# Performance work log

Hardware: AMD Instinct MI355X
Metric: run time of the kernel (lower is better)

The kernel has to match this reference:

```python
import jax, jax.numpy as jnp
import numpy as np

PAD_ID = 0    # scibert [PAD]
SEP_ID = 103  # scibert [SEP]
IGNORE = 100


def setup_inputs() -> dict:
    key = jax.random.key(0)
    ks = jax.random.split(key, 8)
    B, S, D, T = 64, 512, 768, 2
    return {
        "sequence_output": jax.random.normal(ks[0], (B, S, D), dtype=jnp.float32),
        "input_ids": jax.random.randint(ks[1], (B, S), 0, 31090, dtype=jnp.int64),
        "labels": jax.random.randint(ks[2], (B, S), 0, 2, dtype=jnp.int64),
        "W": jax.random.normal(ks[3], (T, D), dtype=jnp.float32) * 0.02,
        "b": jax.random.normal(ks[4], (T,), dtype=jnp.float32) * 0.02,
        "start_trans": jax.random.normal(ks[5], (T,), dtype=jnp.float32) * 0.1,
        "end_trans": jax.random.normal(ks[6], (T,), dtype=jnp.float32) * 0.1,
        "trans": jax.random.normal(ks[7], (T, T), dtype=jnp.float32) * 0.1,
    }


def _crf_llh_token_mean(em, tags, start, end, trans):
    # em: [B,S,T], tags: [B,S]; mask=None in torchcrf => all-ones mask.
    B, S, T = em.shape
    # numerator: score of the gold path
    em_tag = jnp.take_along_axis(em, tags[..., None], axis=2)[..., 0]        # [B,S]
    tr_tag = trans[tags[:, :-1], tags[:, 1:]]                                 # [B,S-1]
    score = start[tags[:, 0]] + em_tag.sum(1) + tr_tag.sum(1) + end[tags[:, -1]]
    # denominator: forward algorithm over time (scan over S-1 tiny steps)
    alpha0 = start[None, :] + em[:, 0]                                        # [B,T]
    em_rest = jnp.swapaxes(em[:, 1:], 0, 1)                                   # [S-1,B,T]

    def step(alpha, em_t):
        # alpha[b,i] + trans[i,j] + em_t[b,j] -> logsumexp over i
        nxt = jax.nn.logsumexp(alpha[:, :, None] + trans[None], axis=1) + em_t
        return nxt, None

    alpha, _ = jax.lax.scan(step, alpha0, em_rest)
    logZ = jax.nn.logsumexp(alpha + end[None, :], axis=1)                     # [B]
    llh = score - logZ
    # reduction='token_mean' with all-ones mask -> sum / (B*S)
    return llh.sum() / jnp.float32(B * S)


def _crf_viterbi(em, start, end, trans):
    # em: [B,S,T] -> decoded tags [B,S] int32
    B, S, T = em.shape
    score0 = start[None, :] + em[:, 0]                                        # [B,T]
    em_rest = jnp.swapaxes(em[:, 1:], 0, 1)                                   # [S-1,B,T]

    def vstep(score, em_t):
        cand = score[:, :, None] + trans[None] + em_t[:, None, :]             # [B,T,T]
        return cand.max(axis=1), cand.argmax(axis=1).astype(jnp.int32)

    final, hist = jax.lax.scan(vstep, score0, em_rest)                        # hist [S-1,B,T]
    final = final + end[None, :]
    last = jnp.argmax(final, axis=1).astype(jnp.int32)                        # [B]

    def back(tag, bp_t):
        prev = jnp.take_along_axis(bp_t, tag[:, None], axis=1)[:, 0]
        return prev, prev

    _, prevs = jax.lax.scan(back, last, hist, reverse=True)                   # [S-1,B]
    tags = jnp.concatenate([prevs, last[None, :]], axis=0)                    # [S,B]
    return jnp.swapaxes(tags, 0, 1)                                           # [B,S]


def reference(sequence_output, input_ids, labels, W, b, start_trans, end_trans, trans):
    mask = (input_ids != PAD_ID) & (input_ids != SEP_ID) & (labels != IGNORE)  # [B,S] bool
    seq = sequence_output * mask[..., None].astype(sequence_output.dtype)
    labels_m = labels * mask.astype(labels.dtype)
    # probablities = relu(hidden2tag(seq))
    em = jax.nn.relu(jnp.einsum("bsd,td->bst", seq, W) + b)                    # [B,S,2]
    loss = _crf_llh_token_mean(em, labels_m, start_trans, end_trans, trans)
    target_emissions = _crf_viterbi(em, start_trans, end_trans, trans).astype(jnp.float32)
    return (loss, target_emissions, labels_m, mask)
```

## Files before the change

### kernel.cpp

```cpp
#include <hip/hip_runtime.h>

#define BB 64
#define SS 512
#define DD 768
#define NROWS (BB*SS)
#define NEG (-1e30f)

__global__ __launch_bounds__(256) void k_emissions(
    const float* __restrict__ seq,
    const int*   __restrict__ input_ids,
    const int*   __restrict__ labels,
    const float* __restrict__ W,
    const float* __restrict__ bias,
    float* __restrict__ em_t,
    int*   __restrict__ tags_t,
    float* __restrict__ out)
{
    const int lane = threadIdx.x & 63;
    const int wid  = blockIdx.x * 4 + (threadIdx.x >> 6);
    const int base = wid * 4;

    const float4* W4 = (const float4*)W;
    float4 w0[3], w1[3];
#pragma unroll
    for (int j = 0; j < 3; ++j) {
        w0[j] = W4[j*64 + lane];
        w1[j] = W4[192 + j*64 + lane];
    }
    const float b0 = bias[0], b1 = bias[1];

    const float4* s4 = (const float4*)seq;
    float4 v[4][3];
#pragma unroll
    for (int r = 0; r < 4; ++r)
#pragma unroll
        for (int j = 0; j < 3; ++j)
            v[r][j] = s4[(size_t)(base + r)*192 + j*64 + lane];

    float d0[4], d1[4];
#pragma unroll
    for (int r = 0; r < 4; ++r) {
        float a0 = 0.f, a1 = 0.f;
#pragma unroll
        for (int j = 0; j < 3; ++j) {
            float4 x = v[r][j];
            a0 += x.x*w0[j].x + x.y*w0[j].y + x.z*w0[j].z + x.w*w0[j].w;
            a1 += x.x*w1[j].x + x.y*w1[j].y + x.z*w1[j].z + x.w*w1[j].w;
        }
        d0[r] = a0; d1[r] = a1;
    }
#pragma unroll
    for (int m = 32; m >= 1; m >>= 1) {
#pragma unroll
        for (int r = 0; r < 4; ++r) {
            d0[r] += __shfl_xor(d0[r], m, 64);
            d1[r] += __shfl_xor(d1[r], m, 64);
        }
    }
    if (lane == 0) {
        const int4 idv = *(const int4*)(input_ids + base);
        const int4 lbv = *(const int4*)(labels + base);
        const int ida[4] = {idv.x, idv.y, idv.z, idv.w};
        const int lba[4] = {lbv.x, lbv.y, lbv.z, lbv.w};
#pragma unroll
        for (int r = 0; r < 4; ++r) {
            const int row = base + r;
            const int id = ida[r], lab = lba[r];
            const int msk = (id != 0 && id != 103 && lab != 100) ? 1 : 0;
            const int lm  = lab * msk;
            const float e0 = fmaxf((msk ? d0[r] : 0.f) + b0, 0.f);
            const float e1 = fmaxf((msk ? d1[r] : 0.f) + b1, 0.f);
            const int b_ = row >> 9, s_ = row & 511;
            *(float2*)(em_t + (s_*BB + b_)*2) = make_float2(e0, e1);
            tags_t[s_*BB + b_] = lm;
            out[1 + NROWS   + row] = (float)lm;
            out[1 + 2*NROWS + row] = (float)msk;
        }
    }
}

__device__ __forceinline__ float lse2(float x, float y) {
    float m = fmaxf(x, y);
    float d = fminf(x, y) - m;
    return m + __logf(1.f + __expf(d));
}

__global__ __launch_bounds__(512) void k_crf(
    const float* __restrict__ em_t,
    const int*   __restrict__ tags_t,
    const float* __restrict__ start,
    const float* __restrict__ endt,
    const float* __restrict__ trans,
    float* __restrict__ out)
{
    __shared__ float4 logP4[8][64];
    __shared__ float4 vitP4[8][64];
    __shared__ float  scoreP[8][64];
    __shared__ float2 vbound[8][64];
    __shared__ unsigned char last_tag_sh[64];
    __shared__ unsigned int  bp_sh[64*33];
    __shared__ unsigned char tags_sh[64*516];

    const int tid  = threadIdx.x;
    const int lane = tid & 63;
    const int wv   = tid >> 6;
    const float t00 = trans[0], t01 = trans[1], t10 = trans[2], t11 = trans[3];
    const float s0 = start[0], s1 = start[1];
    const float e0 = endt[0],  e1 = endt[1];
    const float2* em2 = (const float2*)em_t;

    {
        const int b = lane, c = wv;
        const int k0 = c * 64;
        float2 emv = em2[k0*64 + b];
        int    tg  = tags_t[k0*64 + b];
        float P00,P01,P10,P11, V00,V01,V10,V11, score;
        if (c == 0) {
            P00 = 0.f; P01 = NEG; P10 = NEG; P11 = 0.f;
            V00 = 0.f; V01 = NEG; V10 = NEG; V11 = 0.f;
            score = tg ? (s1 + emv.y) : (s0 + emv.x);
        } else {
            int pt = tags_t[(k0-1)*64 + b];
            P00 = t00 + emv.x; P01 = t01 + emv.y;
            P10 = t10 + emv.x; P11 = t11 + emv.y;
            V00 = P00; V01 = P01; V10 = P10; V11 = P11;
            score = (pt ? (tg ? t11 : t10) : (tg ? t01 : t00))
                  + (tg ? emv.y : emv.x);
        }
        int ptag = tg;

        float2 eb[21]; int tb[21];
#pragma unroll
        for (int i = 0; i < 21; ++i) {
            int kp = k0 + 1 + i;
            eb[i] = em2[kp*64 + b];
            tb[i] = tags_t[kp*64 + b];
        }
#pragma unroll
        for (int jb = 0; jb < 3; ++jb) {
#pragma unroll
            for (int i = 0; i < 21; ++i) {
                const int k = k0 + 1 + jb*21 + i;
                float2 em = eb[i]; int tag = tb[i];
                int kp = k + 21; if (kp > 511) kp = 511;
                eb[i] = em2[kp*64 + b];
                tb[i] = tags_t[kp*64 + b];

                float x0 = lse2(P00 + t00, P01 + t10) + em.x;
                float x1 = lse2(P00 + t01, P01 + t11) + em.y;
                float x2 = lse2(P10 + t00, P11 + t10) + em.x;
                float x3 = lse2(P10 + t01, P11 + t11) + em.y;
                P00 = x0; P01 = x1; P10 = x2; P11 = x3;

                float m0 = fmaxf(V00 + t00, V01 + t10) + em.x;
                float m1 = fmaxf(V00 + t01, V01 + t11) + em.y;
                float m2 = fmaxf(V10 + t00, V11 + t10) + em.x;
                float m3 = fmaxf(V10 + t01, V11 + t11) + em.y;
                V00 = m0; V01 = m1; V10 = m2; V11 = m3;

                score += (ptag ? (tag ? t11 : t10) : (tag ? t01 : t00))
                       + (tag ? em.y : em.x);
                ptag = tag;
            }
        }
        logP4[c][b] = make_float4(P00, P01, P10, P11);
        vitP4[c][b] = make_float4(V00, V01, V10, V11);
        scoreP[c][b] = score;
    }
    __syncthreads();

    if (wv == 0) {
        const int b = lane;
        float2 em0v = em2[b];
        float a0 = s0 + em0v.x, a1 = s1 + em0v.y;
        float sc = 0.f;
#pragma unroll
        for (int c = 0; c < 8; ++c) {
            float4 P = logP4[c][b];
            float n0 = lse2(a0 + P.x, a1 + P.z);
            float n1 = lse2(a0 + P.y, a1 + P.w);
            a0 = n0; a1 = n1;
            sc += scoreP[c][b];
        }
        int tagL = tags_t[511*64 + b];
        sc += tagL ? e1 : e0;
        float logZ = lse2(a0 + e0, a1 + e1);
        float llh = sc - logZ;
#pragma unroll
        for (int m = 32; m >= 1; m >>= 1) llh += __shfl_xor(llh, m, 64);
        if (lane == 0) out[0] = llh / (float)NROWS;
    } else if (wv == 1) {
        const int b = lane;
        float2 em0v = em2[b];
        float v0 = s0 + em0v.x, v1 = s1 + em0v.y;
        vbound[0][b] = make_float2(v0, v1);
#pragma unroll
        for (int c = 0; c < 8; ++c) {
            float4 V = vitP4[c][b];
            float n0 = fmaxf(v0 + V.x, v1 + V.z);
            float n1 = fmaxf(v0 + V.y, v1 + V.w);
            v0 = n0; v1 = n1;
            if (c < 7) vbound[c+1][b] = make_float2(v0, v1);
        }
        int last = (v1 + e1 > v0 + e0) ? 1 : 0;
        last_tag_sh[b] = (unsigned char)last;
        tags_sh[b*516 + 511] = (unsigned char)last;
    }
    __syncthreads();

    {
        const int b = lane, c = wv;
        const int k0 = c * 64;
        float2 vb = vbound[c][b];
        float v0 = vb.x, v1 = vb.y;
        unsigned int acc = 0;

        float2 eb[16];
#pragma unroll
        for (int i = 0; i < 16; ++i) eb[i] = em2[(k0 + i)*64 + b];
#pragma unroll
        for (int jb = 0; jb < 4; ++jb) {
#pragma unroll
            for (int i = 0; i < 16; ++i) {
                const int k = k0 + jb*16 + i;
                float2 em = eb[i];
                int kp = k + 16; if (kp > 511) kp = 511;
                eb[i] = em2[kp*64 + b];
                if (k > 0) {
                    float c00 = v0 + t00, c10 = v1 + t10;
                    float c01 = v0 + t01, c11 = v1 + t11;
                    int bp0 = (c10 > c00);
                    int bp1 = (c11 > c01);
                    v0 = fmaxf(c00, c10) + em.x;
                    v1 = fmaxf(c01, c11) + em.y;
                    acc |= (unsigned)(bp0 | (bp1 << 1)) << (2*(k & 15));
                }
                if ((k & 15) == 15) { bp_sh[b*33 + (k >> 4)] = acc; acc = 0; }
            }
        }
    }
    __syncthreads();

    if (wv == 0) {
        const int b = lane;
        int tag = last_tag_sh[b];
        for (int w = 31; w >= 0; --w) {
            unsigned int word = bp_sh[b*33 + w];
#pragma unroll
            for (int i = 15; i >= 0; --i) {
                const int k = w*16 + i;
                if (k >= 1) {
                    int prev = (word >> ((2*i) | tag)) & 1;
                    tags_sh[b*516 + (k-1)] = (unsigned char)prev;
                    tag = prev;
                }
            }
        }
    }
    __syncthreads();

    for (int idx = tid; idx < NROWS; idx += 512) {
        out[1 + idx] = (float)tags_sh[(idx >> 9)*516 + (idx & 511)];
    }
}

extern "C" void kernel_launch(void* const* d_in, const int* in_sizes, int n_in,
                              void* d_out, int out_size, void* d_ws, size_t ws_size,
                              hipStream_t stream) {
    const float* seq    = (const float*)d_in[0];
    const int*   ids    = (const int*)  d_in[1];
    const int*   labels = (const int*)  d_in[2];
    const float* W      = (const float*)d_in[3];
    const float* bias   = (const float*)d_in[4];
    const float* start  = (const float*)d_in[5];
    const float* endt   = (const float*)d_in[6];
    const float* trans  = (const float*)d_in[7];
    float* out = (float*)d_out;

    float* em_t   = (float*)d_ws;
    int*   tags_t = (int*)((char*)d_ws + (size_t)65536*sizeof(float));

    k_emissions<<<2048, 256, 0, stream>>>(seq, ids, labels, W, bias, em_t, tags_t, out);
    k_crf<<<1, 512, 0, stream>>>(em_t, tags_t, start, endt, trans, out);
}
```

Before: 198.2 us.

## Split CRF into two blocks and use 16 chunks of 32 steps

The CRF kernel now runs as two 1024-thread blocks. Block 0 computes the forward-algorithm log-likelihood and block 1 runs Viterbi with backpointers and backtrace, so the two recurrences proceed in parallel. The chunked scan uses 16 chunks of 32 timesteps instead of 8 chunks of 64, which shortens each thread's serial chain but doubles the cross-chunk combine length. Decoded tags are stored as packed bits in shared memory rather than bytes. The prefetch ring is replaced with batched loads of 8 timesteps.

```diff
diff --git a/kernel.cpp b/kernel.cpp
--- a/kernel.cpp
+++ b/kernel.cpp
@@ -5,6 +5,8 @@
 #define DD 768
 #define NROWS (BB*SS)
 #define NEG (-1e30f)
+#define NCH 16
+#define CL  32
 
 __global__ __launch_bounds__(256) void k_emissions(
     const float* __restrict__ seq,
@@ -85,7 +87,35 @@
     return m + __logf(1.f + __expf(d));
 }
 
-__global__ __launch_bounds__(512) void k_crf(
+#define STEP_L(e_, g_) do { \
+    float n0 = lse2(P00 + t00, P01 + t10) + (e_).x; \
+    float n1 = lse2(P00 + t01, P01 + t11) + (e_).y; \
+    float n2 = lse2(P10 + t00, P11 + t10) + (e_).x; \
+    float n3 = lse2(P10 + t01, P11 + t11) + (e_).y; \
+    P00 = n0; P01 = n1; P10 = n2; P11 = n3; \
+    score += (ptag ? ((g_) ? t11 : t10) : ((g_) ? t01 : t00)) \
+           + ((g_) ? (e_).y : (e_).x); \
+    ptag = (g_); \
+} while (0)
+
+#define STEP_VP(e_) do { \
+    float n0 = fmaxf(V00 + t00, V01 + t10) + (e_).x; \
+    float n1 = fmaxf(V00 + t01, V01 + t11) + (e_).y; \
+    float n2 = fmaxf(V10 + t00, V11 + t10) + (e_).x; \
+    float n3 = fmaxf(V10 + t01, V11 + t11) + (e_).y; \
+    V00 = n0; V01 = n1; V10 = n2; V11 = n3; \
+} while (0)
+
+#define STEP_BP(k_, e_) do { \
+    float c00 = v0 + t00, c10 = v1 + t10; \
+    float c01 = v0 + t01, c11 = v1 + t11; \
+    int bp0 = (c10 > c00); int bp1 = (c11 > c01); \
+    v0 = fmaxf(c00, c10) + (e_).x; v1 = fmaxf(c01, c11) + (e_).y; \
+    acc |= (unsigned)(bp0 | (bp1 << 1)) << (2 * ((k_) & 15)); \
+    if ((((k_) & 15)) == 15) { bp_sh[b*33 + ((k_) >> 4)] = acc; acc = 0u; } \
+} while (0)
+
+__global__ __launch_bounds__(1024) void k_crf(
     const float* __restrict__ em_t,
     const int*   __restrict__ tags_t,
     const float* __restrict__ start,
@@ -93,174 +123,158 @@
     const float* __restrict__ trans,
     float* __restrict__ out)
 {
-    __shared__ float4 logP4[8][64];
-    __shared__ float4 vitP4[8][64];
-    __shared__ float  scoreP[8][64];
-    __shared__ float2 vbound[8][64];
-    __shared__ unsigned char last_tag_sh[64];
-    __shared__ unsigned int  bp_sh[64*33];
-    __shared__ unsigned char tags_sh[64*516];
-
-    const int tid  = threadIdx.x;
-    const int lane = tid & 63;
-    const int wv   = tid >> 6;
+    __shared__ float4 logP4[NCH][BB];
+    __shared__ float  scoreP[NCH][BB];
+    __shared__ float4 vitP4[NCH][BB];
+    __shared__ float2 vbound[NCH][BB];
+    __shared__ unsigned int bp_sh[BB*33];
+    __shared__ unsigned int tagbits[BB*17];
+
+    const int tid = threadIdx.x;
+    const int b   = tid & 63;
+    const int c   = tid >> 6;
+    const int k0  = c * CL;
     const float t00 = trans[0], t01 = trans[1], t10 = trans[2], t11 = trans[3];
     const float s0 = start[0], s1 = start[1];
-    const float e0 = endt[0],  e1 = endt[1];
+    const float en0 = endt[0], en1 = endt[1];
     const float2* em2 = (const float2*)em_t;
 
-    {
-        const int b = lane, c = wv;
-        const int k0 = c * 64;
-        float2 emv = em2[k0*64 + b];
-        int    tg  = tags_t[k0*64 + b];
-        float P00,P01,P10,P11, V00,V01,V10,V11, score;
+    if (blockIdx.x == 0) {
+        float2 e[8]; int g[8];
+        float P00, P01, P10, P11, score; int ptag;
+#pragma unroll
+        for (int i = 0; i < 8; ++i) {
+            e[i] = em2[(k0+i)*BB + b];
+            g[i] = tags_t[(k0+i)*BB + b];
+        }
         if (c == 0) {
             P00 = 0.f; P01 = NEG; P10 = NEG; P11 = 0.f;
+            score = g[0] ? (s1 + e[0].y) : (s0 + e[0].x);
+        } else {
+            int pt = tags_t[(k0-1)*BB + b];
+            P00 = t00 + e[0].x; P01 = t01 + e[0].y;
+            P10 = t10 + e[0].x; P11 = t11 + e[0].y;
+            score = (pt ? (g[0] ? t11 : t10) : (g[0] ? t01 : t00))
+                  + (g[0] ? e[0].y : e[0].x);
+        }
+        ptag = g[0];
+#pragma unroll
+        for (int i = 1; i < 8; ++i) STEP_L(e[i], g[i]);
+#pragma unroll
+        for (int j = 1; j < 4; ++j) {
+#pragma unroll
+            for (int i = 0; i < 8; ++i) {
+                e[i] = em2[(k0 + j*8 + i)*BB + b];
+                g[i] = tags_t[(k0 + j*8 + i)*BB + b];
+            }
+#pragma unroll
+            for (int i = 0; i < 8; ++i) STEP_L(e[i], g[i]);
+        }
+        logP4[c][b] = make_float4(P00, P01, P10, P11);
+        scoreP[c][b] = score;
+        __syncthreads();
+        if (c == 0) {
+            float2 em0v = em2[b];
+            float a0 = s0 + em0v.x, a1 = s1 + em0v.y, sc = 0.f;
+#pragma unroll
+            for (int cc = 0; cc < NCH; ++cc) {
+                float4 P = logP4[cc][b];
+                float n0 = lse2(a0 + P.x, a1 + P.z);
+                float n1 = lse2(a0 + P.y, a1 + P.w);
+                a0 = n0; a1 = n1;
+                sc += scoreP[cc][b];
+            }
+            int tagL = tags_t[511*BB + b];
+            sc += tagL ? en1 : en0;
+            float logZ = lse2(a0 + en0, a1 + en1);
+            float llh = sc - logZ;
+#pragma unroll
+            for (int m = 32; m >= 1; m >>= 1) llh += __shfl_xor(llh, m, 64);
+            if (b == 0) out[0] = llh / (float)NROWS;
+        }
+    } else {
+        float2 e[8];
+        float V00, V01, V10, V11;
+#pragma unroll
+        for (int i = 0; i < 8; ++i) e[i] = em2[(k0+i)*BB + b];
+        if (c == 0) {
             V00 = 0.f; V01 = NEG; V10 = NEG; V11 = 0.f;
-            score = tg ? (s1 + emv.y) : (s0 + emv.x);
         } else {
-            int pt = tags_t[(k0-1)*64 + b];
-            P00 = t00 + emv.x; P01 = t01 + emv.y;
-            P10 = t10 + emv.x; P11 = t11 + emv.y;
-            V00 = P00; V01 = P01; V10 = P10; V11 = P11;
-            score = (pt ? (tg ? t11 : t10) : (tg ? t01 : t00))
-                  + (tg ? emv.y : emv.x);
-        }
-        int ptag = tg;
-
-        float2 eb[21]; int tb[21];
-#pragma unroll
-        for (int i = 0; i < 21; ++i) {
-            int kp = k0 + 1 + i;
-            eb[i] = em2[kp*64 + b];
-            tb[i] = tags_t[kp*64 + b];
-        }
-#pragma unroll
-        for (int jb = 0; jb < 3; ++jb) {
-#pragma unroll
-            for (int i = 0; i < 21; ++i) {
-                const int k = k0 + 1 + jb*21 + i;
-                float2 em = eb[i]; int tag = tb[i];
-                int kp = k + 21; if (kp > 511) kp = 511;
-                eb[i] = em2[kp*64 + b];
-                tb[i] = tags_t[kp*64 + b];
-
-                float x0 = lse2(P00 + t00, P01 + t10) + em.x;
-                float x1 = lse2(P00 + t01, P01 + t11) + em.y;
-                float x2 = lse2(P10 + t00, P11 + t10) + em.x;
-                float x3 = lse2(P10 + t01, P11 + t11) + em.y;
-                P00 = x0; P01 = x1; P10 = x2; P11 = x3;
-
-                float m0 = fmaxf(V00 + t00, V01 + t10) + em.x;
-                float m1 = fmaxf(V00 + t01, V01 + t11) + em.y;
-                float m2 = fmaxf(V10 + t00, V11 + t10) + em.x;
-                float m3 = fmaxf(V10 + t01, V11 + t11) + em.y;
-                V00 = m0; V01 = m1; V10 = m2; V11 = m3;
-
-                score += (ptag ? (tag ? t11 : t10) : (tag ? t01 : t00))
-                       + (tag ? em.y : em.x);
-                ptag = tag;
-            }
-        }
-        logP4[c][b] = make_float4(P00, P01, P10, P11);
+            V00 = t00 + e[0].x; V01 = t01 + e[0].y;
+            V10 = t10 + e[0].x; V11 = t11 + e[0].y;
+        }
+#pragma unroll
+        for (int i = 1; i < 8; ++i) STEP_VP(e[i]);
+#pragma unroll
+        for (int j = 1; j < 4; ++j) {
+#pragma unroll
+            for (int i = 0; i < 8; ++i) e[i] = em2[(k0 + j*8 + i)*BB + b];
+#pragma unroll
+            for (int i = 0; i < 8; ++i) STEP_VP(e[i]);
+        }
         vitP4[c][b] = make_float4(V00, V01, V10, V11);
-        scoreP[c][b] = score;
-    }
-    __syncthreads();
-
-    if (wv == 0) {
-        const int b = lane;
-        float2 em0v = em2[b];
-        float a0 = s0 + em0v.x, a1 = s1 + em0v.y;
-        float sc = 0.f;
-#pragma unroll
-        for (int c = 0; c < 8; ++c) {
-            float4 P = logP4[c][b];
-            float n0 = lse2(a0 + P.x, a1 + P.z);
-            float n1 = lse2(a0 + P.y, a1 + P.w);
-            a0 = n0; a1 = n1;
-            sc += scoreP[c][b];
-        }
-        int tagL = tags_t[511*64 + b];
-        sc += tagL ? e1 : e0;
-        float logZ = lse2(a0 + e0, a1 + e1);
-        float llh = sc - logZ;
-#pragma unroll
-        for (int m = 32; m >= 1; m >>= 1) llh += __shfl_xor(llh, m, 64);
-        if (lane == 0) out[0] = llh / (float)NROWS;
-    } else if (wv == 1) {
-        const int b = lane;
-        float2 em0v = em2[b];
-        float v0 = s0 + em0v.x, v1 = s1 + em0v.y;
-        vbound[0][b] = make_float2(v0, v1);
-#pragma unroll
-        for (int c = 0; c < 8; ++c) {
-            float4 V = vitP4[c][b];
-            float n0 = fmaxf(v0 + V.x, v1 + V.z);
-            float n1 = fmaxf(v0 + V.y, v1 + V.w);
-            v0 = n0; v1 = n1;
-            if (c < 7) vbound[c+1][b] = make_float2(v0, v1);
-        }
-        int last = (v1 + e1 > v0 + e0) ? 1 : 0;
-        last_tag_sh[b] = (unsigned char)last;
-        tags_sh[b*516 + 511] = (unsigned char)last;
-    }
-    __syncthreads();
-
-    {
-        const int b = lane, c = wv;
-        const int k0 = c * 64;
-        float2 vb = vbound[c][b];
-        float v0 = vb.x, v1 = vb.y;
-        unsigned int acc = 0;
-
-        float2 eb[16];
-#pragma unroll
-        for (int i = 0; i < 16; ++i) eb[i] = em2[(k0 + i)*64 + b];
-#pragma unroll
-        for (int jb = 0; jb < 4; ++jb) {
-#pragma unroll
-            for (int i = 0; i < 16; ++i) {
-                const int k = k0 + jb*16 + i;
-                float2 em = eb[i];
-                int kp = k + 16; if (kp > 511) kp = 511;
-                eb[i] = em2[kp*64 + b];
-                if (k > 0) {
-                    float c00 = v0 + t00, c10 = v1 + t10;
-                    float c01 = v0 + t01, c11 = v1 + t11;
-                    int bp0 = (c10 > c00);
-                    int bp1 = (c11 > c01);
-                    v0 = fmaxf(c00, c10) + em.x;
-                    v1 = fmaxf(c01, c11) + em.y;
-                    acc |= (unsigned)(bp0 | (bp1 << 1)) << (2*(k & 15));
-                }
-                if ((k & 15) == 15) { bp_sh[b*33 + (k >> 4)] = acc; acc = 0; }
-            }
-        }
-    }
-    __syncthreads();
-
-    if (wv == 0) {
-        const int b = lane;
-        int tag = last_tag_sh[b];
-        for (int w = 31; w >= 0; --w) {
-            unsigned int word = bp_sh[b*33 + w];
-#pragma unroll
-            for (int i = 15; i >= 0; --i) {
-                const int k = w*16 + i;
-                if (k >= 1) {
-                    int prev = (word >> ((2*i) | tag)) & 1;
-                    tags_sh[b*516 + (k-1)] = (unsigned char)prev;
+        __syncthreads();
+
+        int last = 0;
+        if (c == 0) {
+            float2 em0v = em2[b];
+            float v0 = s0 + em0v.x, v1 = s1 + em0v.y;
+            vbound[0][b] = make_float2(v0, v1);
+#pragma unroll
+            for (int cc = 0; cc < NCH; ++cc) {
+                float4 V = vitP4[cc][b];
+                float n0 = fmaxf(v0 + V.x, v1 + V.z);
+                float n1 = fmaxf(v0 + V.y, v1 + V.w);
+                v0 = n0; v1 = n1;
+                if (cc < NCH-1) vbound[cc+1][b] = make_float2(v0, v1);
+            }
+            last = (v1 + en1 > v0 + en0) ? 1 : 0;
+        }
+        __syncthreads();
+
+        {
+            float2 vb = vbound[c][b];
+            float v0 = vb.x, v1 = vb.y;
+            unsigned acc = 0u;
+#pragma unroll
+            for (int i = 0; i < 8; ++i) e[i] = em2[(k0+i)*BB + b];
+            if (c != 0) STEP_BP(k0, e[0]);
+#pragma unroll
+            for (int i = 1; i < 8; ++i) STEP_BP(k0 + i, e[i]);
+#pragma unroll
+            for (int j = 1; j < 4; ++j) {
+#pragma unroll
+                for (int i = 0; i < 8; ++i) e[i] = em2[(k0 + j*8 + i)*BB + b];
+#pragma unroll
+                for (int i = 0; i < 8; ++i) STEP_BP(k0 + j*8 + i, e[i]);
+            }
+        }
+        __syncthreads();
+
+        if (c == 0) {
+            int tag = last;
+            unsigned acc = ((unsigned)tag) << 31;
+            for (int w = 31; w >= 0; --w) {
+                unsigned word = bp_sh[b*33 + w];
+                const int kbase = w * 16;
+#pragma unroll
+                for (int i = 15; i >= 0; --i) {
+                    if (kbase + i == 0) continue;
+                    int prev = (word >> (2*i + tag)) & 1;
+                    int pos = kbase + i - 1;
+                    acc |= (unsigned)prev << (pos & 31);
+                    if ((pos & 31) == 0) { tagbits[b*17 + (pos >> 5)] = acc; acc = 0u; }
                     tag = prev;
                 }
             }
         }
-    }
-    __syncthreads();
-
-    for (int idx = tid; idx < NROWS; idx += 512) {
-        out[1 + idx] = (float)tags_sh[(idx >> 9)*516 + (idx & 511)];
+        __syncthreads();
+
+        for (int idx = tid; idx < NROWS; idx += 1024) {
+            const int bq = idx >> 9, k = idx & 511;
+            unsigned wd = tagbits[bq*17 + (k >> 5)];
+            out[1 + idx] = (float)((wd >> (k & 31)) & 1);
+        }
     }
 }
 
@@ -281,5 +295,5 @@
     int*   tags_t = (int*)((char*)d_ws + (size_t)65536*sizeof(float));
 
     k_emissions<<<2048, 256, 0, stream>>>(seq, ids, labels, W, bias, em_t, tags_t, out);
-    k_crf<<<1, 512, 0, stream>>>(em_t, tags_t, start, endt, trans, out);
-}
+    k_crf<<<2, 1024, 0, stream>>>(em_t, tags_t, start, endt, trans, out);
+}
```

Measured after the change: 183.1 us. 1.08x faster.
